# Kernel tuning notes

Measured on AMD Instinct MI355X. Metric: run time of the kernel, lower is better.

## Reference

```python
import jax, jax.numpy as jnp
import numpy as np

# Dimensions (match init_kwargs / input_specs)
B, S, D = 4, 2048, 1024
H, DK = 16, 64
CL = 64            # chunk_len
C, N, NL = 32, 2, 128  # chunks, neighbors, neighbor_len
EPS = 1e-5
SCALE = 1.0 / np.sqrt(DK)


def setup_inputs() -> dict:
    key = jax.random.key(0)
    ks = jax.random.split(key, 8)
    w_in = 1.0 / np.sqrt(D)   # xavier-like scale for projections
    return {
        "h": jax.random.normal(ks[0], (B, S, D), jnp.float32),
        "e": jax.random.normal(ks[1], (B, C, N, NL, D), jnp.float32),
        "ln_g": jnp.ones((D,), jnp.float32),
        "ln_b": jnp.zeros((D,), jnp.float32),
        "Wq": jax.random.normal(ks[2], (D, H * DK), jnp.float32) * w_in,
        "bq": jnp.zeros((H * DK,), jnp.float32),
        "Wk": jax.random.normal(ks[3], (D, H * DK), jnp.float32) * w_in,
        "bk": jnp.zeros((H * DK,), jnp.float32),
        "Wv": jax.random.normal(ks[4], (D, H * DK), jnp.float32) * w_in,
        "bv": jnp.zeros((H * DK,), jnp.float32),
        "Wo": jax.random.normal(ks[5], (H * DK, D), jnp.float32) * (1.0 / np.sqrt(H * DK)),
        "bo": jnp.zeros((D,), jnp.float32),
    }


def _layernorm(x, g, b):
    mu = jnp.mean(x, axis=-1, keepdims=True)
    var = jnp.mean(jnp.square(x - mu), axis=-1, keepdims=True)
    return (x - mu) * jax.lax.rsqrt(var + EPS) * g + b


def reference(h, e, ln_g, ln_b, Wq, bq, Wk, bk, Wv, bv, Wo, bo):
    residual = h
    # shift queries so each chunk attends to neighbors retrieved for the previous chunk
    hs = _layernorm(h[:, CL - 1:], ln_g, ln_b)          # [B, S-CL+1, D]
    total = C * CL
    pad = max(0, total - hs.shape[1])
    hp = jnp.pad(hs, ((0, 0), (0, pad), (0, 0))) if pad > 0 else hs[:, :total]
    hb = hp.reshape(B, C, CL, D)                         # [B,C,CL,D]

    q = (hb @ Wq + bq).reshape(B, C, CL, H, DK)
    k = (e @ Wk + bk).reshape(B, C, N, NL, H, DK)
    v = (e @ Wv + bv).reshape(B, C, N, NL, H, DK)

    # scores: [B, C, H, CL, N, NL], softmax over merged (N, NL)
    attn = jnp.einsum('bcihd,bcnjhd->bchinj', q, k) * SCALE
    sh = attn.shape
    attn = jax.nn.softmax(attn.reshape(sh[0], sh[1], sh[2], sh[3], -1), axis=-1).reshape(sh)

    o = jnp.einsum('bchinj,bcnjhd->bcihd', attn, v).reshape(B, C * CL, H * DK)
    o = o @ Wo + bo                                      # [B, C*CL, D]
    # shift output back and crop to original length
    o = jnp.pad(o, ((0, 0), (CL - 1, 0), (0, 0)))[:, :S]
    return o + residual
```

## Files before the change

kernel.cpp:

```cpp
#include <hip/hip_runtime.h>


typedef __attribute__((ext_vector_type(8))) short short8;
typedef __attribute__((ext_vector_type(4))) float f32x4;
typedef unsigned short ushort_t;
typedef unsigned long long u64;

__device__ inline ushort_t f2bf(float f) {
  union { float f; unsigned int u; } v; v.f = f;
  unsigned int u = v.u;
  return (ushort_t)((u + 0x7fffu + ((u >> 16) & 1u)) >> 16);
}
__device__ inline float bf2f(ushort_t s) {
  union { unsigned int u; float f; } v; v.u = ((unsigned int)s) << 16;
  return v.f;
}

__device__ inline void gl_lds16(const void* g, void* l) {
  __builtin_amdgcn_global_load_lds(
      (const __attribute__((address_space(1))) unsigned int*)g,
      (__attribute__((address_space(3))) unsigned int*)l, 16, 0, 0);
}

__global__ void prep_kernel(const float* __restrict__ W0, const float* __restrict__ W1,
                            const float* __restrict__ W2, const float* __restrict__ W3,
                            ushort_t* __restrict__ T0, ushort_t* __restrict__ T1,
                            ushort_t* __restrict__ T2, ushort_t* __restrict__ T3,
                            const float* __restrict__ h, const float* __restrict__ lg,
                            const float* __restrict__ lb, ushort_t* __restrict__ hb,
                            const float* __restrict__ e, ushort_t* __restrict__ e_bf) {
  __shared__ float tile[32][33];
  __shared__ float red[8];
  const int blk = blockIdx.x, t = threadIdx.x;

  if (blk < 4096) {
    const int z = blk >> 10, xy = blk & 1023;
    const float* W = (z == 0) ? W0 : (z == 1) ? W1 : (z == 2) ? W2 : W3;
    ushort_t* WT   = (z == 0) ? T0 : (z == 1) ? T1 : (z == 2) ? T2 : T3;
    int k0 = (xy & 31) * 32, n0 = (xy >> 5) * 32;
    int c = t & 31, r = t >> 5;
#pragma unroll
    for (int p = 0; p < 4; p++)
      tile[r + p * 8][c] = W[(size_t)(k0 + r + p * 8) * 1024 + n0 + c];
    __syncthreads();
#pragma unroll
    for (int p = 0; p < 4; p++)
      WT[(size_t)(n0 + r + p * 8) * 1024 + k0 + c] = f2bf(tile[c][r + p * 8]);
    return;
  }
  if (blk < 12288) {
    int row = blk - 4096;
    int b = row >> 11, jj = row & 2047;
    ushort_t* dst = hb + (size_t)row * 1024;
    if (jj >= 1985) {
      ((unsigned int*)dst)[t] = 0u;
      ((unsigned int*)dst)[t + 256] = 0u;
      return;
    }
    const float* src = h + ((size_t)(b << 11) + jj + 63) * 1024;
    f32x4 x = *(const f32x4*)&src[t * 4];
    float s = x[0] + x[1] + x[2] + x[3];
    float sq = x[0]*x[0] + x[1]*x[1] + x[2]*x[2] + x[3]*x[3];
#pragma unroll
    for (int off = 32; off > 0; off >>= 1) {
      s  += __shfl_xor(s, off);
      sq += __shfl_xor(sq, off);
    }
    if ((t & 63) == 0) { red[(t >> 6) * 2] = s; red[(t >> 6) * 2 + 1] = sq; }
    __syncthreads();
    float sum = red[0] + red[2] + red[4] + red[6];
    float sumsq = red[1] + red[3] + red[5] + red[7];
    float mu = sum * (1.f / 1024.f);
    float var = sumsq * (1.f / 1024.f) - mu * mu;
    float rs = rsqrtf(var + 1e-5f);
    f32x4 gg = *(const f32x4*)&lg[t * 4];
    f32x4 bv = *(const f32x4*)&lb[t * 4];
    ushort_t o0 = f2bf((x[0] - mu) * rs * gg[0] + bv[0]);
    ushort_t o1 = f2bf((x[1] - mu) * rs * gg[1] + bv[1]);
    ushort_t o2 = f2bf((x[2] - mu) * rs * gg[2] + bv[2]);
    ushort_t o3 = f2bf((x[3] - mu) * rs * gg[3] + bv[3]);
    u64 pack = (u64)o0 | ((u64)o1 << 16) | ((u64)o2 << 32) | ((u64)o3 << 48);
    *(u64*)&dst[t * 4] = pack;
    return;
  }
  {
    int i = (blk - 12288) * 256 + t;
    const f32x4* sp = (const f32x4*)(e + (size_t)i * 8);
    f32x4 a = sp[0], b = sp[1];
    short8 o;
    o[0] = (short)f2bf(a[0]); o[1] = (short)f2bf(a[1]);
    o[2] = (short)f2bf(a[2]); o[3] = (short)f2bf(a[3]);
    o[4] = (short)f2bf(b[0]); o[5] = (short)f2bf(b[1]);
    o[6] = (short)f2bf(b[2]); o[7] = (short)f2bf(b[3]);
    *(short8*)(e_bf + (size_t)i * 8) = o;
  }
}

template <int EPI>
__launch_bounds__(256, 2)
__global__ void gemm_bt(const ushort_t* __restrict__ A, const ushort_t* __restrict__ BT,
                        const float* __restrict__ bias, ushort_t* __restrict__ Cb,
                        float* __restrict__ Cf, const float* __restrict__ resid) {
  const int bid = blockIdx.x;
  if (EPI == 1 && bid >= 512) {
    int tt = bid - 512;
    int b = tt / 63, r = tt % 63;
    size_t idx = ((size_t)(b * 2048) + r) * 1024 + threadIdx.x * 4;
    *(f32x4*)&Cf[idx] = *(const f32x4*)&resid[idx];
    return;
  }
  __shared__ __attribute__((aligned(16))) ushort_t lds[32768];
  const int cpx = 64;
  const int swz = (bid & 7) * cpx + (bid >> 3);
  const int tm = (swz >> 3) * 128, tn = (swz & 7) * 128;
  const int t = threadIdx.x, lane = t & 63, wv = t >> 6;
  const int wm = (wv >> 1) * 64, wn = (wv & 1) * 64;
  const int row16 = lane & 15, g = lane >> 4;

  const int c0 = t, c1 = t + 256;
  const int ra0 = c0 >> 2, sa0 = ((c0 & 3) ^ ((ra0 >> 1) & 3)) * 8;
  const int ra1 = c1 >> 2, sa1 = ((c1 & 3) ^ ((ra1 >> 1) & 3)) * 8;
  const ushort_t* Ag0 = A + (size_t)(tm + ra0) * 1024 + sa0;
  const ushort_t* Ag1 = A + (size_t)(tm + ra1) * 1024 + sa1;
  const ushort_t* Bg0 = BT + (size_t)(tn + ra0) * 1024 + sa0;
  const ushort_t* Bg1 = BT + (size_t)(tn + ra1) * 1024 + sa1;

#define STG_A(T) { ushort_t* L_ = lds + ((T) & 3) * 8192; const int k0_ = (T) * 32; \
    gl_lds16(Ag0 + k0_, L_ + c0 * 8); gl_lds16(Ag1 + k0_, L_ + c1 * 8); }
#define STG_B(T) { ushort_t* L_ = lds + ((T) & 3) * 8192; const int k0_ = (T) * 32; \
    gl_lds16(Bg0 + k0_, L_ + 4096 + c0 * 8); gl_lds16(Bg1 + k0_, L_ + 4096 + c1 * 8); }

  int aoff[4], boff[4];
#pragma unroll
  for (int m = 0; m < 4; m++) {
    int ra = wm + m * 16 + row16;
    aoff[m] = ra * 32 + (g ^ ((ra >> 1) & 3)) * 8;
  }
#pragma unroll
  for (int n = 0; n < 4; n++) {
    int rb = wn + n * 16 + row16;
    boff[n] = 4096 + rb * 32 + (g ^ ((rb >> 1) & 3)) * 8;
  }

  f32x4 acc[4][4] = {};
  STG_A(0); STG_B(0); STG_A(1); STG_B(1);
  for (int T = 0; T < 32; ++T) {
    const ushort_t* Lb = lds + (T & 3) * 8192;
    if (T < 31) { asm volatile("s_waitcnt vmcnt(4)" ::: "memory"); }
    else        { asm volatile("s_waitcnt vmcnt(0)" ::: "memory"); }
    __builtin_amdgcn_s_barrier();
    short8 af0, af1;
    short8 bfv[4];
#pragma unroll
    for (int n = 0; n < 4; n++) bfv[n] = *(const short8*)&Lb[boff[n]];
    af0 = *(const short8*)&Lb[aoff[0]];
    af1 = *(const short8*)&Lb[aoff[1]];
    if (T < 30) STG_A(T + 2);
    __builtin_amdgcn_s_barrier();
    asm volatile("s_waitcnt lgkmcnt(0)" ::: "memory");
    __builtin_amdgcn_sched_barrier(0);
    __builtin_amdgcn_s_setprio(1);
#pragma unroll
    for (int n = 0; n < 4; n++) {
      acc[0][n] = __builtin_amdgcn_mfma_f32_16x16x32_bf16(af0, bfv[n], acc[0][n], 0, 0, 0);
      acc[1][n] = __builtin_amdgcn_mfma_f32_16x16x32_bf16(af1, bfv[n], acc[1][n], 0, 0, 0);
    }
    __builtin_amdgcn_s_setprio(0);
    __builtin_amdgcn_s_barrier();
    af0 = *(const short8*)&Lb[aoff[2]];
    af1 = *(const short8*)&Lb[aoff[3]];
    if (T < 30) STG_B(T + 2);
    __builtin_amdgcn_s_barrier();
    asm volatile("s_waitcnt lgkmcnt(0)" ::: "memory");
    __builtin_amdgcn_sched_barrier(0);
    __builtin_amdgcn_s_setprio(1);
#pragma unroll
    for (int n = 0; n < 4; n++) {
      acc[2][n] = __builtin_amdgcn_mfma_f32_16x16x32_bf16(af0, bfv[n], acc[2][n], 0, 0, 0);
      acc[3][n] = __builtin_amdgcn_mfma_f32_16x16x32_bf16(af1, bfv[n], acc[3][n], 0, 0, 0);
    }
    __builtin_amdgcn_s_setprio(0);
  }
#undef STG_A
#undef STG_B

  const int cr = g * 4, cc = row16;
  if (EPI == 0) {
    const int cb = tn + wn;
    float bsv[4];
#pragma unroll
    for (int n = 0; n < 4; n++) bsv[n] = bias[cb + n * 16 + cc];
#pragma unroll
    for (int m = 0; m < 4; m++) {
      int rbase = tm + wm + m * 16 + cr;
#pragma unroll
      for (int j = 0; j < 4; j++) {
        u64 pack = (u64)f2bf(acc[m][0][j] + bsv[0])
                 | ((u64)f2bf(acc[m][1][j] + bsv[1]) << 16)
                 | ((u64)f2bf(acc[m][2][j] + bsv[2]) << 32)
                 | ((u64)f2bf(acc[m][3][j] + bsv[3]) << 48);
        *(u64*)&Cb[(size_t)(rbase + j) * 1024 + cb + cc * 4] = pack;
      }
    }
  } else {
#pragma unroll
    for (int m = 0; m < 4; m++) {
#pragma unroll
      for (int n = 0; n < 4; n++) {
        int col = tn + wn + n * 16 + cc;
        float bsv = bias[col];
#pragma unroll
        for (int j = 0; j < 4; j++) {
          int rg = tm + wm + m * 16 + cr + j;
          float v = acc[m][n][j] + bsv;
          int b = rg >> 11, jj = rg & 2047;
          if (jj < 1985) {
            size_t oi = ((size_t)(b << 11) + jj + 63) * 1024 + col;
            Cf[oi] = v + resid[oi];
          }
        }
      }
    }
  }
}

__launch_bounds__(512, 2)
__global__ void kv_attn(const ushort_t* __restrict__ A, const ushort_t* __restrict__ WkvT,
                        const float* __restrict__ bk, const float* __restrict__ bv,
                        const ushort_t* __restrict__ Qb, ushort_t* __restrict__ Ob) {
  __shared__ __attribute__((aligned(16))) ushort_t smem[75776];
  ushort_t* lds = smem;
  const int bid = blockIdx.x;
  const int swz = (bid & 7) * 128 + (bid >> 3);
  const int bc = swz >> 3, hp = swz & 7;
  const int tm = bc * 256;
  const int t = threadIdx.x, lane = t & 63, wv = t >> 6;
  const int wm = wv >> 2, wn = wv & 3;
  const int row16 = lane & 15, g = lane >> 4;

  {
    const int hb2q = t >> 8, tlq = t & 255;
    ushort_t* QsH = smem + 67584 + hb2q * 4096;
    size_t qbase = ((size_t)bc * 64) * 1024 + (hp * 2 + hb2q) * 64;
    int ch = tlq, r = ch >> 3, gq = (ch & 7) ^ (r & 7);
    gl_lds16(Qb + qbase + (size_t)r * 1024 + gq * 8, &QsH[ch * 8]);
    ch = tlq + 256; r = ch >> 3; gq = (ch & 7) ^ (r & 7);
    gl_lds16(Qb + qbase + (size_t)r * 1024 + gq * 8, &QsH[ch * 8]);
  }

  const ushort_t* Agp[4];
  const ushort_t* Bgp[4];
  int destC[4];
#pragma unroll
  for (int p = 0; p < 4; p++) {
    int c = t + 512 * p;
    int r = c >> 3, s = c & 7;
    int srck = (s ^ (r & 7)) * 8;
    destC[p] = c * 8;
    Agp[p] = A + (size_t)(tm + r) * 1024 + srck;
    int grow = (r < 128) ? (hp * 128 + r) : (1024 + hp * 128 + (r - 128));
    Bgp[p] = WkvT + (size_t)grow * 1024 + srck;
  }
#define STG64(T) { ushort_t* L_ = lds + ((T) & 1) * 32768; const int k0_ = (T) * 64; \
    gl_lds16(Agp[0] + k0_, L_ + destC[0]); gl_lds16(Agp[1] + k0_, L_ + destC[1]); \
    gl_lds16(Agp[2] + k0_, L_ + destC[2]); gl_lds16(Agp[3] + k0_, L_ + destC[3]); \
    gl_lds16(Bgp[0] + k0_, L_ + 16384 + destC[0]); gl_lds16(Bgp[1] + k0_, L_ + 16384 + destC[1]); \
    gl_lds16(Bgp[2] + k0_, L_ + 16384 + destC[2]); gl_lds16(Bgp[3] + k0_, L_ + 16384 + destC[3]); }

  int aoffk[2][8], boffk[2][4];
#pragma unroll
  for (int kk2 = 0; kk2 < 2; kk2++) {
#pragma unroll
    for (int m = 0; m < 8; m++) {
      int ra = wm * 128 + m * 16 + row16;
      aoffk[kk2][m] = ra * 64 + (((g + 4 * kk2)) ^ (ra & 7)) * 8;
    }
#pragma unroll
    for (int n = 0; n < 4; n++) {
      int rb = wn * 64 + n * 16 + row16;
      boffk[kk2][n] = 16384 + rb * 64 + (((g + 4 * kk2)) ^ (rb & 7)) * 8;
    }
  }

  f32x4 acc[8][4] = {};
  STG64(0);
  for (int T = 0; T < 16; ++T) {
    asm volatile("s_waitcnt vmcnt(0)" ::: "memory");
    __builtin_amdgcn_s_barrier();
    if (T < 15) STG64(T + 1);
    const ushort_t* Lb = lds + (T & 1) * 32768;
#pragma unroll
    for (int kk2 = 0; kk2 < 2; kk2++) {
      short8 af[8], bfv[4];
#pragma unroll
      for (int n = 0; n < 4; n++) bfv[n] = *(const short8*)&Lb[boffk[kk2][n]];
#pragma unroll
      for (int m = 0; m < 8; m++) af[m] = *(const short8*)&Lb[aoffk[kk2][m]];
      __builtin_amdgcn_s_setprio(1);
#pragma unroll
      for (int m = 0; m < 8; m++)
#pragma unroll
        for (int n = 0; n < 4; n++)
          acc[m][n] = __builtin_amdgcn_mfma_f32_16x16x32_bf16(af[m], bfv[n], acc[m][n], 0, 0, 0);
      __builtin_amdgcn_s_setprio(0);
    }
  }
#undef STG64

  __syncthreads();

  if (wn < 2) {
    ushort_t* KsH = smem + wn * 16896;
    float bsv[4];
#pragma unroll
    for (int n = 0; n < 4; n++) bsv[n] = bk[hp * 128 + wn * 64 + n * 16 + row16];
#pragma unroll
    for (int m = 0; m < 8; m++) {
      int krow0 = wm * 128 + m * 16 + g * 4;
#pragma unroll
      for (int j = 0; j < 4; j++) {
        int krow = krow0 + j;
        u64 pack = (u64)f2bf(acc[m][0][j] + bsv[0])
                 | ((u64)f2bf(acc[m][1][j] + bsv[1]) << 16)
                 | ((u64)f2bf(acc[m][2][j] + bsv[2]) << 32)
                 | ((u64)f2bf(acc[m][3][j] + bsv[3]) << 48);
        int sl = ((row16 >> 1) ^ (krow & 7)) * 8 + (row16 & 1) * 4;
        *(u64*)&KsH[krow * 64 + sl] = pack;
      }
    }
  } else {
    ushort_t* VtH = smem + 33792 + (wn & 1) * 16896;
    float bsv[4];
#pragma unroll
    for (int n = 0; n < 4; n++) bsv[n] = bv[hp * 128 + (wn - 2) * 64 + n * 16 + row16];
#pragma unroll
    for (int m = 0; m < 8; m++) {
      int krow0 = wm * 128 + m * 16 + g * 4;
#pragma unroll
      for (int n = 0; n < 4; n++) {
        int od = n * 16 + row16;
        u64 pack = (u64)f2bf(acc[m][n][0] + bsv[n])
                 | ((u64)f2bf(acc[m][n][1] + bsv[n]) << 16)
                 | ((u64)f2bf(acc[m][n][2] + bsv[n]) << 32)
                 | ((u64)f2bf(acc[m][n][3] + bsv[n]) << 48);
        *(u64*)&VtH[od * 264 + krow0] = pack;
      }
    }
  }
  __syncthreads();

  const int tl = t & 255, hb2 = t >> 8;
  const int wvL = tl >> 6, laneL = tl & 63;
  ushort_t* QsH = smem + 67584 + hb2 * 4096;
  ushort_t* KsH = smem + hb2 * 16896;
  ushort_t* SpH = KsH;
  ushort_t* VtH = smem + 33792 + hb2 * 16896;

  const int rowA = laneL & 15, kgA = (laneL >> 4) * 8;
  const int cswz = (rowA & 7) << 3;
  f32x4 accs[4][4] = {};
#pragma unroll
  for (int kk = 0; kk < 64; kk += 32) {
    int cq = ((kk + kgA) ^ cswz);
    short8 af[4], bfr[4];
#pragma unroll
    for (int m = 0; m < 4; m++) af[m] = *(const short8*)&QsH[(m * 16 + rowA) * 64 + cq];
#pragma unroll
    for (int n = 0; n < 4; n++)
      bfr[n] = *(const short8*)&KsH[(wvL * 64 + n * 16 + rowA) * 64 + cq];
#pragma unroll
    for (int m = 0; m < 4; m++)
#pragma unroll
      for (int n = 0; n < 4; n++)
        accs[m][n] = __builtin_amdgcn_mfma_f32_16x16x32_bf16(af[m], bfr[n], accs[m][n], 0, 0, 0);
  }
  __syncthreads();

  {
    const int cr = (laneL >> 4) * 4, cc = laneL & 15;
#pragma unroll
    for (int m = 0; m < 4; m++)
#pragma unroll
      for (int n = 0; n < 4; n++)
#pragma unroll
        for (int j = 0; j < 4; j++)
          SpH[(m * 16 + cr + j) * 264 + wvL * 64 + n * 16 + cc] = f2bf(accs[m][n][j]);
  }
  __syncthreads();

  {
    const int r = tl >> 2, q = tl & 3;
    const int base = r * 264 + q * 64;
    float ev[64];
#pragma unroll
    for (int p = 0; p < 8; p++) {
      short8 sv = *(const short8*)&SpH[base + p * 8];
#pragma unroll
      for (int i = 0; i < 8; i++) ev[p * 8 + i] = bf2f((ushort_t)sv[i]);
    }
    float mx = ev[0];
#pragma unroll
    for (int i = 1; i < 64; i++) mx = fmaxf(mx, ev[i]);
    mx = fmaxf(mx, __shfl_xor(mx, 1));
    mx = fmaxf(mx, __shfl_xor(mx, 2));
    float sum = 0.f;
#pragma unroll
    for (int i = 0; i < 64; i++) {
      ev[i] = __expf((ev[i] - mx) * 0.125f);
      sum += ev[i];
    }
    sum += __shfl_xor(sum, 1);
    sum += __shfl_xor(sum, 2);
    float inv = 1.f / sum;
#pragma unroll
    for (int p = 0; p < 8; p++) {
      short8 pv;
#pragma unroll
      for (int i = 0; i < 8; i++) pv[i] = (short)f2bf(ev[p * 8 + i] * inv);
      *(short8*)&SpH[base + p * 8] = pv;
    }
  }
  __syncthreads();

  {
    f32x4 acco[4] = {};
#pragma unroll
    for (int kt = 0; kt < 8; kt++) {
      short8 bfv = *(const short8*)&VtH[(wvL * 16 + rowA) * 264 + kt * 32 + kgA];
#pragma unroll
      for (int m = 0; m < 4; m++) {
        short8 af = *(const short8*)&SpH[(m * 16 + rowA) * 264 + kt * 32 + kgA];
        acco[m] = __builtin_amdgcn_mfma_f32_16x16x32_bf16(af, bfv, acco[m], 0, 0, 0);
      }
    }
    const int cr = (laneL >> 4) * 4, cc = laneL & 15;
    size_t obase = ((size_t)bc * 64) * 1024 + (hp * 2 + hb2) * 64 + wvL * 16 + cc;
#pragma unroll
    for (int m = 0; m < 4; m++)
#pragma unroll
      for (int j = 0; j < 4; j++)
        Ob[obase + (size_t)(m * 16 + cr + j) * 1024] = f2bf(acco[m][j]);
  }
}

extern "C" void kernel_launch(void* const* d_in, const int* in_sizes, int n_in,
                              void* d_out, int out_size, void* d_ws, size_t ws_size,
                              hipStream_t stream) {
  const float* h    = (const float*)d_in[0];
  const float* e    = (const float*)d_in[1];
  const float* ln_g = (const float*)d_in[2];
  const float* ln_b = (const float*)d_in[3];
  const float* Wq   = (const float*)d_in[4];
  const float* bq   = (const float*)d_in[5];
  const float* Wk   = (const float*)d_in[6];
  const float* bk   = (const float*)d_in[7];
  const float* Wv   = (const float*)d_in[8];
  const float* bv   = (const float*)d_in[9];
  const float* Wo   = (const float*)d_in[10];
  const float* bo   = (const float*)d_in[11];
  float* out = (float*)d_out;

  char* ws = (char*)d_ws;
  const size_t MB = 1024 * 1024;
  ushort_t* WqT  = (ushort_t*)(ws + 0 * MB);
  ushort_t* WkT  = (ushort_t*)(ws + 2 * MB);
  ushort_t* WvT  = (ushort_t*)(ws + 4 * MB);
  ushort_t* WoT  = (ushort_t*)(ws + 6 * MB);
  ushort_t* hb   = (ushort_t*)(ws + 8 * MB);
  ushort_t* e_bf = (ushort_t*)(ws + 24 * MB);
  ushort_t* Qb   = (ushort_t*)(ws + 88 * MB);
  ushort_t* Obuf = (ushort_t*)(ws + 104 * MB);

  prep_kernel<<<28672, 256, 0, stream>>>(Wq, Wk, Wv, Wo, WqT, WkT, WvT, WoT,
                                         h, ln_g, ln_b, hb, e, e_bf);

  gemm_bt<0><<<512, 256, 0, stream>>>(hb, WqT, bq, Qb, nullptr, nullptr);
  kv_attn<<<1024, 512, 0, stream>>>(e_bf, WkT, bk, bv, Qb, Obuf);

  gemm_bt<1><<<764, 256, 0, stream>>>(Obuf, WoT, bo, nullptr, out, h);
}
```

Before: 249.3 us.

## Use BK=64 double-buffered LDS staging with 8-way XOR swizzle in GEMM

Replaces the 4-stage K=32 pipeline, which interleaved A/B staging with half-tile MFMA bursts and several barriers per step, with a 2-stage double buffer of K=64 tiles. The new loop waits on all outstanding loads, issues a single barrier, prefetches the next tile and runs 32 MFMAs. The LDS swizzle becomes an 8-chunk XOR to match the wider rows. This halves the number of loop iterations and barriers, but the prefetch distance drops to one tile and the vmcnt(0) wait can expose global load latency.

```diff
diff --git a/kernel.cpp b/kernel.cpp
--- a/kernel.cpp
+++ b/kernel.cpp
@@ -117,72 +117,63 @@
   const int wm = (wv >> 1) * 64, wn = (wv & 1) * 64;
   const int row16 = lane & 15, g = lane >> 4;
 
-  const int c0 = t, c1 = t + 256;
-  const int ra0 = c0 >> 2, sa0 = ((c0 & 3) ^ ((ra0 >> 1) & 3)) * 8;
-  const int ra1 = c1 >> 2, sa1 = ((c1 & 3) ^ ((ra1 >> 1) & 3)) * 8;
-  const ushort_t* Ag0 = A + (size_t)(tm + ra0) * 1024 + sa0;
-  const ushort_t* Ag1 = A + (size_t)(tm + ra1) * 1024 + sa1;
-  const ushort_t* Bg0 = BT + (size_t)(tn + ra0) * 1024 + sa0;
-  const ushort_t* Bg1 = BT + (size_t)(tn + ra1) * 1024 + sa1;
-
-#define STG_A(T) { ushort_t* L_ = lds + ((T) & 3) * 8192; const int k0_ = (T) * 32; \
-    gl_lds16(Ag0 + k0_, L_ + c0 * 8); gl_lds16(Ag1 + k0_, L_ + c1 * 8); }
-#define STG_B(T) { ushort_t* L_ = lds + ((T) & 3) * 8192; const int k0_ = (T) * 32; \
-    gl_lds16(Bg0 + k0_, L_ + 4096 + c0 * 8); gl_lds16(Bg1 + k0_, L_ + 4096 + c1 * 8); }
-
-  int aoff[4], boff[4];
-#pragma unroll
-  for (int m = 0; m < 4; m++) {
-    int ra = wm + m * 16 + row16;
-    aoff[m] = ra * 32 + (g ^ ((ra >> 1) & 3)) * 8;
-  }
-#pragma unroll
-  for (int n = 0; n < 4; n++) {
-    int rb = wn + n * 16 + row16;
-    boff[n] = 4096 + rb * 32 + (g ^ ((rb >> 1) & 3)) * 8;
+  const ushort_t* Agp[4];
+  const ushort_t* Bgp[4];
+  int destC[4];
+#pragma unroll
+  for (int p = 0; p < 4; p++) {
+    int c = t + 256 * p;
+    int r = c >> 3, s = c & 7;
+    int srck = (s ^ (r & 7)) * 8;
+    destC[p] = c * 8;
+    Agp[p] = A + (size_t)(tm + r) * 1024 + srck;
+    Bgp[p] = BT + (size_t)(tn + r) * 1024 + srck;
+  }
+#define STGBT(T) { ushort_t* L_ = lds + ((T) & 1) * 16384; const int k0_ = (T) * 64; \
+    gl_lds16(Agp[0] + k0_, L_ + destC[0]); gl_lds16(Agp[1] + k0_, L_ + destC[1]); \
+    gl_lds16(Agp[2] + k0_, L_ + destC[2]); gl_lds16(Agp[3] + k0_, L_ + destC[3]); \
+    gl_lds16(Bgp[0] + k0_, L_ + 8192 + destC[0]); gl_lds16(Bgp[1] + k0_, L_ + 8192 + destC[1]); \
+    gl_lds16(Bgp[2] + k0_, L_ + 8192 + destC[2]); gl_lds16(Bgp[3] + k0_, L_ + 8192 + destC[3]); }
+
+  int aoffk[2][4], boffk[2][4];
+#pragma unroll
+  for (int kk2 = 0; kk2 < 2; kk2++) {
+#pragma unroll
+    for (int m = 0; m < 4; m++) {
+      int ra = wm + m * 16 + row16;
+      aoffk[kk2][m] = ra * 64 + (((g + 4 * kk2)) ^ (ra & 7)) * 8;
+    }
+#pragma unroll
+    for (int n = 0; n < 4; n++) {
+      int rb = wn + n * 16 + row16;
+      boffk[kk2][n] = 8192 + rb * 64 + (((g + 4 * kk2)) ^ (rb & 7)) * 8;
+    }
   }
 
   f32x4 acc[4][4] = {};
-  STG_A(0); STG_B(0); STG_A(1); STG_B(1);
-  for (int T = 0; T < 32; ++T) {
-    const ushort_t* Lb = lds + (T & 3) * 8192;
-    if (T < 31) { asm volatile("s_waitcnt vmcnt(4)" ::: "memory"); }
-    else        { asm volatile("s_waitcnt vmcnt(0)" ::: "memory"); }
+  STGBT(0);
+  for (int T = 0; T < 16; ++T) {
+    asm volatile("s_waitcnt vmcnt(0)" ::: "memory");
     __builtin_amdgcn_s_barrier();
-    short8 af0, af1;
-    short8 bfv[4];
-#pragma unroll
-    for (int n = 0; n < 4; n++) bfv[n] = *(const short8*)&Lb[boff[n]];
-    af0 = *(const short8*)&Lb[aoff[0]];
-    af1 = *(const short8*)&Lb[aoff[1]];
-    if (T < 30) STG_A(T + 2);
-    __builtin_amdgcn_s_barrier();
-    asm volatile("s_waitcnt lgkmcnt(0)" ::: "memory");
-    __builtin_amdgcn_sched_barrier(0);
-    __builtin_amdgcn_s_setprio(1);
-#pragma unroll
-    for (int n = 0; n < 4; n++) {
-      acc[0][n] = __builtin_amdgcn_mfma_f32_16x16x32_bf16(af0, bfv[n], acc[0][n], 0, 0, 0);
-      acc[1][n] = __builtin_amdgcn_mfma_f32_16x16x32_bf16(af1, bfv[n], acc[1][n], 0, 0, 0);
-    }
-    __builtin_amdgcn_s_setprio(0);
-    __builtin_amdgcn_s_barrier();
-    af0 = *(const short8*)&Lb[aoff[2]];
-    af1 = *(const short8*)&Lb[aoff[3]];
-    if (T < 30) STG_B(T + 2);
-    __builtin_amdgcn_s_barrier();
-    asm volatile("s_waitcnt lgkmcnt(0)" ::: "memory");
-    __builtin_amdgcn_sched_barrier(0);
-    __builtin_amdgcn_s_setprio(1);
-#pragma unroll
-    for (int n = 0; n < 4; n++) {
-      acc[2][n] = __builtin_amdgcn_mfma_f32_16x16x32_bf16(af0, bfv[n], acc[2][n], 0, 0, 0);
-      acc[3][n] = __builtin_amdgcn_mfma_f32_16x16x32_bf16(af1, bfv[n], acc[3][n], 0, 0, 0);
-    }
-    __builtin_amdgcn_s_setprio(0);
-  }
-#undef STG_A
-#undef STG_B
+    if (T < 15) STGBT(T + 1);
+    const ushort_t* Lb = lds + (T & 1) * 16384;
+#pragma unroll
+    for (int kk2 = 0; kk2 < 2; kk2++) {
+      short8 af[4], bfv[4];
+#pragma unroll
+      for (int n = 0; n < 4; n++) bfv[n] = *(const short8*)&Lb[boffk[kk2][n]];
+#pragma unroll
+      for (int m = 0; m < 4; m++) af[m] = *(const short8*)&Lb[aoffk[kk2][m]];
+      __builtin_amdgcn_s_setprio(1);
+#pragma unroll
+      for (int m = 0; m < 4; m++)
+#pragma unroll
+        for (int n = 0; n < 4; n++)
+          acc[m][n] = __builtin_amdgcn_mfma_f32_16x16x32_bf16(af[m], bfv[n], acc[m][n], 0, 0, 0);
+      __builtin_amdgcn_s_setprio(0);
+    }
+  }
+#undef STGBT
 
   const int cr = g * 4, cc = row16;
   if (EPI == 0) {
```

New measurement: 246.9 us (median of 2 runs). About the same (-0.9%).
